# Optimization experiments

Measured on AMD Instinct MI355X. Metric: run time of the kernel, lower is better.

Reference implementation:

```python
import jax, jax.numpy as jnp
import numpy as np

B, H, L, D = 4, 4096, 8, 64  # queries shape [B, L, H, D]
FACTOR = 5
U = FACTOR * int(np.ceil(np.log(4096)))  # u_part = u = 45 (L_q == L_k)


def setup_inputs() -> dict:
    key = jax.random.key(0)
    kq, kk, kv, ki = jax.random.split(key, 4)
    queries = jax.random.normal(kq, (4, 4096, 8, 64), dtype=jnp.float32)
    keys = jax.random.normal(kk, (4, 4096, 8, 64), dtype=jnp.float32)
    values = jax.random.normal(kv, (4, 4096, 8, 64), dtype=jnp.float32)
    index_sample = jax.random.randint(ki, (4096, U), 0, 4096)  # torch.randint(key_length,(L_Q,sample_k))
    return {"queries": queries, "keys": keys, "values": values, "index_sample": index_sample}


def reference(queries, keys, values, index_sample):
    # (B, L, H, D) -> (B, H, L, D)
    q = jnp.transpose(queries, (0, 2, 1, 3))
    k = jnp.transpose(keys, (0, 2, 1, 3))
    v = jnp.transpose(values, (0, 2, 1, 3))
    b, h, l_q, d = q.shape
    l_k = k.shape[2]
    n_top = index_sample.shape[1]  # u == u_part == 45 here

    # --- _prob_QK: sampled QK scores (avoid materializing key_expand [B,H,Lq,Lk,D]) ---
    # key_sample: [B, H, Lq, sample_k, D]
    key_sample = k[:, :, index_sample, :]
    # Q_i . K_sampled: [B, H, Lq, sample_k]
    qk_sample = jnp.einsum('bhld,bhlsd->bhls', q, key_sample)
    # sparsity measure M = max - mean(over full key_length)
    m = jnp.max(qk_sample, axis=-1) - jnp.sum(qk_sample, axis=-1) / l_k  # [B,H,Lq]
    _, m_top = jax.lax.top_k(m, n_top)  # [B, H, u]

    # reduced queries: [B, H, u, D]
    q_reduce = jnp.take_along_axis(q, m_top[..., None], axis=2)
    scores_top = jnp.einsum('bhud,bhkd->bhuk', q_reduce, k)  # [B, H, u, Lk]

    scale = 1.0 / jnp.sqrt(jnp.asarray(d, dtype=q.dtype))
    scores_top = scores_top * scale

    # --- _get_initial_context (mask_flag=False): mean of values broadcast over queries ---
    context = jnp.broadcast_to(jnp.mean(v, axis=2, keepdims=True), (b, h, l_q, d))

    # --- _update_context: softmax + scatter attn@V into the top-u query rows ---
    attn = jax.nn.softmax(scores_top, axis=-1)  # [B, H, u, Lk]
    update = jnp.einsum('bhuk,bhkd->bhud', attn, v)  # [B, H, u, D]
    b_idx = jnp.arange(b)[:, None, None]
    h_idx = jnp.arange(h)[None, :, None]
    context = context.at[b_idx, h_idx, m_top].set(update)
    return context  # [B, H, Lq, D]
```

## Files before the change

### kernel.cpp

```cpp
#include <hip/hip_runtime.h>
#include <hip/hip_bf16.h>


#define NB 4
#define NH 8
#define NL 4096
#define ND 64
#define NS 45
#define SCALE 0.125f
#define NCHUNK 16
#define CHUNK 256

typedef float floatx4 __attribute__((ext_vector_type(4)));

static __device__ __forceinline__ float neg_inf() { return -__builtin_inff(); }

template <int CTRL>
static __device__ __forceinline__ float dpp_add(float x) {
  int y = __builtin_amdgcn_update_dpp(0, __builtin_bit_cast(int, x), CTRL,
                                      0xF, 0xF, true);
  return x + __builtin_bit_cast(float, y);
}
static __device__ __forceinline__ float red16(float x) {
  x = dpp_add<0x140>(x);
  x = dpp_add<0x141>(x);
  x = dpp_add<0x4E>(x);
  x = dpp_add<0xB1>(x);
  return x;
}

__global__ __launch_bounds__(256) void k_compute_m(
    const float* __restrict__ q, const float* __restrict__ k,
    const int* __restrict__ idxs, float* __restrict__ m_out)
{
  __shared__ int sidx[4][NS];
  int gb = blockIdx.x;
  int pair = gb & 7;
  int b = pair >> 1, hg = pair & 1;
  int lg = gb >> 3;
  int t = threadIdx.x, w = t >> 6, lane = t & 63, g = lane >> 4;
  int l = lg * 4 + w;

  if (lane < NS) sidx[w][lane] = idxs[l * NS + lane];

  const floatx4* q4 =
      (const floatx4*)(q + ((size_t)(b * NL + l) * NH + hg * 4) * ND);
  floatx4 qr = __builtin_nontemporal_load(q4 + lane);

  const floatx4* kb4 = (const floatx4*)k + ((size_t)b * NL * NH + hg * 4) * 16;

  float mx = neg_inf(), sm = 0.f;
#pragma unroll 5
  for (int s = 0; s < NS; ++s) {
    int ki = sidx[w][s];
    floatx4 kk = kb4[(size_t)ki * 128 + lane];
    float p = kk.x * qr.x + kk.y * qr.y + kk.z * qr.z + kk.w * qr.w;
    p = red16(p);
    mx = fmaxf(mx, p);
    sm += p;
  }
  if ((lane & 15) == 0)
    m_out[((size_t)b * NH + hg * 4 + g) * NL + l] = mx - sm * (1.0f / 4096.0f);
}

__global__ __launch_bounds__(256) void k_topk_p1(
    const float* __restrict__ m_in, unsigned long long* __restrict__ cand)
{
  __shared__ unsigned long long keys[512];
  __shared__ unsigned long long wred[4];
  int blk = blockIdx.x;
  int bh = blk >> 3, slice = blk & 7;
  int t = threadIdx.x, wid = t >> 6, lane = t & 63;
  int base = slice * 512;
  for (int i = t; i < 512; i += 256) {
    float v = m_in[bh * NL + base + i];
    unsigned u = __float_as_uint(v);
    u ^= (u >> 31) ? 0xFFFFFFFFu : 0x80000000u;
    keys[i] = ((unsigned long long)u << 32) | (unsigned)(~(unsigned)(base + i));
  }
  __syncthreads();
  for (int it = 0; it < NS; ++it) {
    unsigned long long k0 = keys[t], k1 = keys[t + 256];
    unsigned long long best = k0 > k1 ? k0 : k1;
#pragma unroll
    for (int off = 32; off; off >>= 1) {
      unsigned long long o = __shfl_xor(best, off);
      if (o > best) best = o;
    }
    if (lane == 0) wred[wid] = best;
    __syncthreads();
    if (t == 0) {
      unsigned long long b0 = wred[0];
      if (wred[1] > b0) b0 = wred[1];
      if (wred[2] > b0) b0 = wred[2];
      if (wred[3] > b0) b0 = wred[3];
      cand[blk * NS + it] = b0;
      int gi = (int)(~(unsigned)(b0 & 0xFFFFFFFFull));
      keys[gi - base] = 0;
    }
    __syncthreads();
  }
}

__global__ __launch_bounds__(256) void k_topk_p2(
    const unsigned long long* __restrict__ cand, int* __restrict__ mtop)
{
  __shared__ unsigned long long keys[8 * NS];
  __shared__ unsigned long long wred[4];
  __shared__ unsigned long long sbest;
  int bh = blockIdx.x;
  int t = threadIdx.x, wid = t >> 6, lane = t & 63;
  for (int i = t; i < 8 * NS; i += 256) keys[i] = cand[bh * 8 * NS + i];
  __syncthreads();
  for (int it = 0; it < NS; ++it) {
    unsigned long long best = (t < 8 * NS) ? keys[t] : 0ull;
    if (t + 256 < 8 * NS) {
      unsigned long long k1 = keys[t + 256];
      if (k1 > best) best = k1;
    }
#pragma unroll
    for (int off = 32; off; off >>= 1) {
      unsigned long long o = __shfl_xor(best, off);
      if (o > best) best = o;
    }
    if (lane == 0) wred[wid] = best;
    __syncthreads();
    if (t == 0) {
      unsigned long long b0 = wred[0];
      if (wred[1] > b0) b0 = wred[1];
      if (wred[2] > b0) b0 = wred[2];
      if (wred[3] > b0) b0 = wred[3];
      sbest = b0;
      mtop[bh * NS + it] = (int)(~(unsigned)(b0 & 0xFFFFFFFFull));
    }
    __syncthreads();
    unsigned long long bb = sbest;
    if (t < 8 * NS && keys[t] == bb) keys[t] = 0;
    if (t + 256 < 8 * NS && keys[t + 256] == bb) keys[t + 256] = 0;
    __syncthreads();
  }
}

__global__ __launch_bounds__(256) void k_meanv_part(
    const float* __restrict__ v, float* __restrict__ vpart)
{
  __shared__ float part[4][ND];
  int bh = blockIdx.x, c = blockIdx.y;
  int b = bh >> 3, h = bh & 7;
  int t = threadIdx.x, d = t & 63, g = t >> 6;
  float a0 = 0.f, a1 = 0.f, a2 = 0.f, a3 = 0.f;
  const float* vb = v + ((size_t)(b * NL + c * 64) * NH + h) * ND + d;
#pragma unroll
  for (int i = 0; i < 4; i++) {
    a0 += vb[(size_t)(g + 4 * (4 * i + 0)) * NH * ND];
    a1 += vb[(size_t)(g + 4 * (4 * i + 1)) * NH * ND];
    a2 += vb[(size_t)(g + 4 * (4 * i + 2)) * NH * ND];
    a3 += vb[(size_t)(g + 4 * (4 * i + 3)) * NH * ND];
  }
  part[g][d] = (a0 + a1) + (a2 + a3);
  __syncthreads();
  if (g == 0) {
    float s = part[0][d] + part[1][d] + part[2][d] + part[3][d];
    vpart[(bh * 64 + c) * ND + d] = s;
  }
}

__global__ __launch_bounds__(64) void k_meanv_final(
    const float* __restrict__ vpart, float* __restrict__ meanv)
{
  int bh = blockIdx.x, d = threadIdx.x;
  float s = 0.f;
  for (int c = 0; c < 64; c++) s += vpart[(bh * 64 + c) * ND + d];
  meanv[bh * ND + d] = s * (1.0f / 4096.0f);
}

__global__ __launch_bounds__(256) void k_fill(
    const float* __restrict__ meanv, float4* __restrict__ out4)
{
  const int total = NB * NH * NL * ND / 4;
  const float4* mv4 = (const float4*)meanv;
  for (int i = blockIdx.x * 256 + threadIdx.x; i < total; i += gridDim.x * 256) {
    int bh = i >> 16;
    int d4 = i & 15;
    out4[i] = mv4[bh * 16 + d4];
  }
}

__global__ __launch_bounds__(256) void k_scores(
    const float* __restrict__ q, const float* __restrict__ k,
    const float* __restrict__ v, const int* __restrict__ mtop,
    float* __restrict__ mc_out, float* __restrict__ lc_out,
    float* __restrict__ op_out)
{
  __shared__ float QLDS[NS * ND];
  __shared__ float SLDS[NS * 260];
  __shared__ int mt[NS];
  __shared__ float mcs[NS], lcs[NS];

  int gb = blockIdx.x;
  int xcd = gb & 7, seq = gb >> 3;
  int bh = xcd * 4 + (seq >> 4);
  int c = seq & 15;
  int b = bh >> 3, h = bh & 7;
  int t = threadIdx.x;
  int wid = t >> 6, lane = t & 63;

  if (t < NS) mt[t] = mtop[bh * NS + t];
  __syncthreads();

  const float4* q4 = (const float4*)q;
  float4* QL4 = (float4*)QLDS;
  for (int i = t; i < NS * 16; i += 256) {
    int u = i >> 4, j = i & 15;
    QL4[i] = q4[((size_t)(b * NL + mt[u]) * NH + h) * 16 + j];
  }
  __syncthreads();

  {
    int kk = t;
    const float4* k4 =
        (const float4*)(k + ((size_t)(b * NL + c * CHUNK + kk) * NH + h) * ND);
    float4 kr[16];
#pragma unroll
    for (int j = 0; j < 16; j++) kr[j] = k4[j];
    for (int u = 0; u < NS; ++u) {
      float dot = 0.f;
#pragma unroll
      for (int j = 0; j < 16; j++) {
        float4 qq = QL4[u * 16 + j];
        dot += qq.x * kr[j].x + qq.y * kr[j].y + qq.z * kr[j].z + qq.w * kr[j].w;
      }
      SLDS[u * 260 + kk] = dot * SCALE;
    }
  }
  __syncthreads();

  for (int u = wid; u < NS; u += 4) {
    float4 sv = *(const float4*)&SLDS[u * 260 + lane * 4];
    float mx = fmaxf(fmaxf(sv.x, sv.y), fmaxf(sv.z, sv.w));
#pragma unroll
    for (int off = 32; off; off >>= 1) mx = fmaxf(mx, __shfl_xor(mx, off));
    float e0 = expf(sv.x - mx), e1 = expf(sv.y - mx);
    float e2 = expf(sv.z - mx), e3 = expf(sv.w - mx);
    float s = e0 + e1 + e2 + e3;
#pragma unroll
    for (int off = 32; off; off >>= 1) s += __shfl_xor(s, off);
    *(float4*)&SLDS[u * 260 + lane * 4] = make_float4(e0, e1, e2, e3);
    if (lane == 0) { mcs[u] = mx; lcs[u] = s; }
  }
  __syncthreads();

  float acc[12];
#pragma unroll
  for (int i = 0; i < 12; i++) acc[i] = 0.f;
  const float* vbase = v + ((size_t)(b * NL + c * CHUNK) * NH + h) * ND + lane;
  for (int kb = 0; kb < 64; ++kb) {
    float vd0 = vbase[(size_t)(kb * 4 + 0) * NH * ND];
    float vd1 = vbase[(size_t)(kb * 4 + 1) * NH * ND];
    float vd2 = vbase[(size_t)(kb * 4 + 2) * NH * ND];
    float vd3 = vbase[(size_t)(kb * 4 + 3) * NH * ND];
#pragma unroll
    for (int i = 0; i < 12; i++) {
      int u = wid + 4 * i;
      if (u < NS) {
        float4 p4 = *(const float4*)&SLDS[u * 260 + kb * 4];
        acc[i] += p4.x * vd0 + p4.y * vd1 + p4.z * vd2 + p4.w * vd3;
      }
    }
  }
#pragma unroll
  for (int i = 0; i < 12; i++) {
    int u = wid + 4 * i;
    if (u < NS)
      op_out[(((size_t)bh * NCHUNK + c) * NS + u) * ND + lane] = acc[i];
  }
  if (t < NS) {
    mc_out[(bh * NCHUNK + c) * NS + t] = mcs[t];
    lc_out[(bh * NCHUNK + c) * NS + t] = lcs[t];
  }
}

__global__ __launch_bounds__(256) void k_combine(
    const float* __restrict__ mc, const float* __restrict__ lc,
    const float* __restrict__ op, const int* __restrict__ mtop,
    float* __restrict__ out)
{
  int gw = blockIdx.x * 4 + (threadIdx.x >> 6);
  int lane = threadIdx.x & 63;
  int bh = gw / NS, u = gw % NS;
  float M = neg_inf();
  for (int c = 0; c < NCHUNK; c++)
    M = fmaxf(M, mc[(bh * NCHUNK + c) * NS + u]);
  float Lsum = 0.f, O = 0.f;
  for (int c = 0; c < NCHUNK; c++) {
    float e = expf(mc[(bh * NCHUNK + c) * NS + u] - M);
    Lsum += lc[(bh * NCHUNK + c) * NS + u] * e;
    O += op[(((size_t)bh * NCHUNK + c) * NS + u) * ND + lane] * e;
  }
  int row = mtop[bh * NS + u];
  out[((size_t)bh * NL + row) * ND + lane] = O / Lsum;
}

extern "C" void kernel_launch(void* const* d_in, const int* in_sizes, int n_in,
                              void* d_out, int out_size, void* d_ws, size_t ws_size,
                              hipStream_t stream) {
  const float* q = (const float*)d_in[0];
  const float* k = (const float*)d_in[1];
  const float* v = (const float*)d_in[2];
  const int* idxs = (const int*)d_in[3];
  float* out = (float*)d_out;
  float* ws = (float*)d_ws;

  float* m_ws  = ws;
  int*   mtop  = (int*)(ws + 131072);
  float* meanv = ws + 132512;
  float* mc    = ws + 134560;
  float* lc    = ws + 157600;
  float* op    = ws + 180640;
  float* vpart = op;
  unsigned long long* cand = (unsigned long long*)(op + 131072);

  hipLaunchKernelGGL(k_compute_m,   dim3(8192),      dim3(256), 0, stream, q, k, idxs, m_ws);
  hipLaunchKernelGGL(k_topk_p1,     dim3(256),       dim3(256), 0, stream, m_ws, cand);
  hipLaunchKernelGGL(k_topk_p2,     dim3(32),        dim3(256), 0, stream, cand, mtop);
  hipLaunchKernelGGL(k_meanv_part,  dim3(32, 64),    dim3(256), 0, stream, v, vpart);
  hipLaunchKernelGGL(k_meanv_final, dim3(32),        dim3(64),  0, stream, vpart, meanv);
  hipLaunchKernelGGL(k_fill,        dim3(2048),      dim3(256), 0, stream, meanv, (float4*)out);
  hipLaunchKernelGGL(k_scores,      dim3(512),       dim3(256), 0, stream, q, k, v, mtop, mc, lc, op);
  hipLaunchKernelGGL(k_combine,     dim3(360),       dim3(256), 0, stream, mc, lc, op, mtop, out);
}
```

Measured before the change: 206.2 us.

## Split k_scores work across 1024 threads and make sample index wave-uniform

k_scores now runs with 1024 threads per block. Each key's 64-wide dot product is split across 4 lanes and combined with a DPP reduction, and the softmax and P·V row loops are spread over 16 waves instead of 4. The goal is to cut per-thread register pressure (16 float4 key registers, 12 accumulators) and increase latency hiding in the chunk kernel. In k_compute_m, the sampled key index is read with readfirstlane so it lives in a scalar register. The trade-off is 4x redundant LDS reads of Q and extra reduction instructions.

```diff
diff --git a/kernel.cpp b/kernel.cpp
--- a/kernel.cpp
+++ b/kernel.cpp
@@ -28,6 +28,11 @@
   x = dpp_add<0xB1>(x);
   return x;
 }
+static __device__ __forceinline__ float red4(float x) {
+  x = dpp_add<0xB1>(x);
+  x = dpp_add<0x4E>(x);
+  return x;
+}
 
 __global__ __launch_bounds__(256) void k_compute_m(
     const float* __restrict__ q, const float* __restrict__ k,
@@ -52,7 +57,7 @@
   float mx = neg_inf(), sm = 0.f;
 #pragma unroll 5
   for (int s = 0; s < NS; ++s) {
-    int ki = sidx[w][s];
+    int ki = __builtin_amdgcn_readfirstlane(sidx[w][s]);
     floatx4 kk = kb4[(size_t)ki * 128 + lane];
     float p = kk.x * qr.x + kk.y * qr.y + kk.z * qr.z + kk.w * qr.w;
     p = red16(p);
@@ -186,7 +191,7 @@
   }
 }
 
-__global__ __launch_bounds__(256) void k_scores(
+__global__ __launch_bounds__(1024) void k_scores(
     const float* __restrict__ q, const float* __restrict__ k,
     const float* __restrict__ v, const int* __restrict__ mtop,
     float* __restrict__ mc_out, float* __restrict__ lc_out,
@@ -210,32 +215,34 @@
 
   const float4* q4 = (const float4*)q;
   float4* QL4 = (float4*)QLDS;
-  for (int i = t; i < NS * 16; i += 256) {
-    int u = i >> 4, j = i & 15;
-    QL4[i] = q4[((size_t)(b * NL + mt[u]) * NH + h) * 16 + j];
+  if (t < NS * 16) {
+    int u = t >> 4, j = t & 15;
+    QL4[t] = q4[((size_t)(b * NL + mt[u]) * NH + h) * 16 + j];
   }
   __syncthreads();
 
   {
-    int kk = t;
+    int kk = wid * 16 + (lane >> 2);
+    int seg = lane & 3;
     const float4* k4 =
-        (const float4*)(k + ((size_t)(b * NL + c * CHUNK + kk) * NH + h) * ND);
-    float4 kr[16];
-#pragma unroll
-    for (int j = 0; j < 16; j++) kr[j] = k4[j];
+        (const float4*)(k + ((size_t)(b * NL + c * CHUNK + kk) * NH + h) * ND)
+        + seg * 4;
+    float4 k0 = k4[0], k1 = k4[1], k2 = k4[2], k3 = k4[3];
+    const float4* qp = QL4 + seg * 4;
     for (int u = 0; u < NS; ++u) {
-      float dot = 0.f;
-#pragma unroll
-      for (int j = 0; j < 16; j++) {
-        float4 qq = QL4[u * 16 + j];
-        dot += qq.x * kr[j].x + qq.y * kr[j].y + qq.z * kr[j].z + qq.w * kr[j].w;
-      }
-      SLDS[u * 260 + kk] = dot * SCALE;
-    }
-  }
-  __syncthreads();
-
-  for (int u = wid; u < NS; u += 4) {
+      float4 a0 = qp[u * 16 + 0], a1 = qp[u * 16 + 1];
+      float4 a2 = qp[u * 16 + 2], a3 = qp[u * 16 + 3];
+      float dot = a0.x * k0.x + a0.y * k0.y + a0.z * k0.z + a0.w * k0.w
+                + a1.x * k1.x + a1.y * k1.y + a1.z * k1.z + a1.w * k1.w
+                + a2.x * k2.x + a2.y * k2.y + a2.z * k2.z + a2.w * k2.w
+                + a3.x * k3.x + a3.y * k3.y + a3.z * k3.z + a3.w * k3.w;
+      dot = red4(dot);
+      if (seg == 0) SLDS[u * 260 + kk] = dot * SCALE;
+    }
+  }
+  __syncthreads();
+
+  for (int u = wid; u < NS; u += 16) {
     float4 sv = *(const float4*)&SLDS[u * 260 + lane * 4];
     float mx = fmaxf(fmaxf(sv.x, sv.y), fmaxf(sv.z, sv.w));
 #pragma unroll
@@ -250,9 +257,9 @@
   }
   __syncthreads();
 
-  float acc[12];
-#pragma unroll
-  for (int i = 0; i < 12; i++) acc[i] = 0.f;
+  float acc[3];
+#pragma unroll
+  for (int i = 0; i < 3; i++) acc[i] = 0.f;
   const float* vbase = v + ((size_t)(b * NL + c * CHUNK) * NH + h) * ND + lane;
   for (int kb = 0; kb < 64; ++kb) {
     float vd0 = vbase[(size_t)(kb * 4 + 0) * NH * ND];
@@ -260,8 +267,8 @@
     float vd2 = vbase[(size_t)(kb * 4 + 2) * NH * ND];
     float vd3 = vbase[(size_t)(kb * 4 + 3) * NH * ND];
 #pragma unroll
-    for (int i = 0; i < 12; i++) {
-      int u = wid + 4 * i;
+    for (int i = 0; i < 3; i++) {
+      int u = wid + 16 * i;
       if (u < NS) {
         float4 p4 = *(const float4*)&SLDS[u * 260 + kb * 4];
         acc[i] += p4.x * vd0 + p4.y * vd1 + p4.z * vd2 + p4.w * vd3;
@@ -269,8 +276,8 @@
     }
   }
 #pragma unroll
-  for (int i = 0; i < 12; i++) {
-    int u = wid + 4 * i;
+  for (int i = 0; i < 3; i++) {
+    int u = wid + 16 * i;
     if (u < NS)
       op_out[(((size_t)bh * NCHUNK + c) * NS + u) * ND + lane] = acc[i];
   }
@@ -320,12 +327,12 @@
   float* vpart = op;
   unsigned long long* cand = (unsigned long long*)(op + 131072);
 
-  hipLaunchKernelGGL(k_compute_m,   dim3(8192),      dim3(256), 0, stream, q, k, idxs, m_ws);
-  hipLaunchKernelGGL(k_topk_p1,     dim3(256),       dim3(256), 0, stream, m_ws, cand);
-  hipLaunchKernelGGL(k_topk_p2,     dim3(32),        dim3(256), 0, stream, cand, mtop);
-  hipLaunchKernelGGL(k_meanv_part,  dim3(32, 64),    dim3(256), 0, stream, v, vpart);
-  hipLaunchKernelGGL(k_meanv_final, dim3(32),        dim3(64),  0, stream, vpart, meanv);
-  hipLaunchKernelGGL(k_fill,        dim3(2048),      dim3(256), 0, stream, meanv, (float4*)out);
-  hipLaunchKernelGGL(k_scores,      dim3(512),       dim3(256), 0, stream, q, k, v, mtop, mc, lc, op);
-  hipLaunchKernelGGL(k_combine,     dim3(360),       dim3(256), 0, stream, mc, lc, op, mtop, out);
-}
+  hipLaunchKernelGGL(k_compute_m,   dim3(8192),      dim3(256),  0, stream, q, k, idxs, m_ws);
+  hipLaunchKernelGGL(k_topk_p1,     dim3(256),       dim3(256),  0, stream, m_ws, cand);
+  hipLaunchKernelGGL(k_topk_p2,     dim3(32),        dim3(256),  0, stream, cand, mtop);
+  hipLaunchKernelGGL(k_meanv_part,  dim3(32, 64),    dim3(256),  0, stream, v, vpart);
+  hipLaunchKernelGGL(k_meanv_final, dim3(32),        dim3(64),   0, stream, vpart, meanv);
+  hipLaunchKernelGGL(k_fill,        dim3(2048),      dim3(256),  0, stream, meanv, (float4*)out);
+  hipLaunchKernelGGL(k_scores,      dim3(512),       dim3(1024), 0, stream, q, k, v, mtop, mc, lc, op);
+  hipLaunchKernelGGL(k_combine,     dim3(360),       dim3(256),  0, stream, mc, lc, op, mtop, out);
+}
```

Result: faster. 186.6 us (-9.5%).
